# Kernel tuning notes

Measured on AMD Instinct MI355X. Metric: run time of the kernel, lower is better.

Reference implementation:

```python
import jax, jax.numpy as jnp
import numpy as np

BATCH = 4096
LATENT = 2048
ZDIM = 128
TEMP = 0.5
PRIOR = 0.3
PRIOR_PRIME = 0.5
GAMMA = 1.0
BETA = 0.0
EPS = 1e-8  # torch CosineSimilarity eps


def setup_inputs() -> dict:
    key = jax.random.key(0)
    k = jax.random.split(key, 6)
    return {
        "h_i": jax.random.normal(k[0], (BATCH, LATENT), dtype=jnp.float32),
        "h_j": jax.random.normal(k[1], (BATCH, LATENT), dtype=jnp.float32),
        "z_i": jax.random.normal(k[2], (BATCH, ZDIM), dtype=jnp.float32),
        "z_j": jax.random.normal(k[3], (BATCH, ZDIM), dtype=jnp.float32),
        "target": jax.random.randint(k[4], (BATCH, 1), 0, 2, dtype=jnp.int64 if jax.config.jax_enable_x64 else jnp.int32),
        "W": jax.random.normal(k[5], (1, LATENT), dtype=jnp.float32) * (1.0 / np.sqrt(LATENT)),
        "b": jnp.zeros((1,), dtype=jnp.float32),
        "weight_onnpu": jnp.asarray(0.5, dtype=jnp.float32),
    }


def _onnpu_loss(inp, target):
    # inp: [B, 1] classifier logit; target: [B, 1] in {0, 1} -> {-1, +1}
    t = (target * 2 - 1).astype(inp.dtype)
    positive = (t == 1).astype(inp.dtype)
    unlabeled = (t == -1).astype(inp.dtype)
    one = jnp.asarray(1.0, inp.dtype)
    n_pos = jnp.maximum(one, jnp.sum(positive))
    n_unl = jnp.maximum(one, jnp.sum(unlabeled))
    sig = jax.nn.sigmoid  # loss(x) = sigmoid(-x)
    y_pos = sig(-(positive * inp)) * positive
    y_pos_inv = sig(positive * inp) * positive
    y_unl = sig(unlabeled * inp) * unlabeled
    positive_risk = PRIOR_PRIME / n_pos * jnp.sum(y_pos)
    negative_risk = ((1.0 - PRIOR_PRIME) / (n_unl * (1.0 - PRIOR)) * jnp.sum(y_unl)
                     - (1.0 - PRIOR_PRIME) * PRIOR / (n_pos * (1.0 - PRIOR)) * jnp.sum(y_pos_inv))
    # nnPU correction (nnPU=True, beta=0, gamma=1)
    return jnp.where(negative_risk < -BETA, -GAMMA * negative_risk,
                     positive_risk + negative_risk)


def _nt_xent_loss(z_i, z_j):
    B = z_i.shape[0]
    N = 2 * B
    z = jnp.concatenate([z_i, z_j], axis=0)  # [N, D]
    zn = z / jnp.maximum(jnp.linalg.norm(z, axis=1, keepdims=True), EPS)
    sim = (zn @ zn.T) / TEMP  # [N, N] cosine similarity / temperature
    idx = jnp.arange(N)
    pos = sim[idx, (idx + B) % N]  # positive pair logit per row
    # CE over [positive | all-other-than-self]: denominator is logsumexp over
    # the row with the self-similarity (diagonal) excluded.
    sim_masked = jnp.where(idx[:, None] == idx[None, :], -jnp.inf, sim)
    lse = jax.nn.logsumexp(sim_masked, axis=1)
    return jnp.sum(lse - pos) / N


def reference(h_i, h_j, z_i, z_j, target, W, b, weight_onnpu):
    logit_i = h_i @ W.T + b  # [B, 1]
    logit_j = h_j @ W.T + b
    onnpu_l = 0.5 * (_onnpu_loss(logit_i, target) + _onnpu_loss(logit_j, target))
    nt_xent_l = _nt_xent_loss(z_i, z_j)
    return weight_onnpu * onnpu_l + (1.0 - weight_onnpu) * nt_xent_l
```

## Files before the change

### kernel.cpp

```cpp
#include <hip/hip_runtime.h>

#define BATCH  4096
#define NROWS  8192
#define LATENT 2048
#define ZDIM   128
#define PRIORc       0.3f
#define PRIOR_PRIMEc 0.5f

typedef __attribute__((ext_vector_type(8))) short bf16x8;
typedef __attribute__((ext_vector_type(4))) float f32x4;

__device__ inline unsigned short f2bf_rne(float f) {
    unsigned int u = __float_as_uint(f);
    u = u + 0x7fffu + ((u >> 16) & 1u);
    return (unsigned short)(u >> 16);
}

__device__ inline float wave_reduce_sum(float v) {
#pragma unroll
    for (int m = 1; m < 64; m <<= 1) v += __shfl_xor(v, m, 64);
    return v;
}

#define ZSCALE 1.69864464f

__global__ void k_prep(const float* __restrict__ z_i, const float* __restrict__ z_j,
                       const float* __restrict__ h_i, const float* __restrict__ h_j,
                       const float* __restrict__ W, const float* __restrict__ bb,
                       unsigned short* __restrict__ znb, float* __restrict__ pos,
                       float* __restrict__ dexp, float* __restrict__ S_row,
                       float* __restrict__ logits) {
    int bid = blockIdx.x;
    int wave = threadIdx.x >> 6, lane = threadIdx.x & 63;
    if (bid < 1024) {
        if (threadIdx.x < 8) S_row[bid * 8 + threadIdx.x] = 0.f;
        int r = bid * 4 + wave;
        int p = r + BATCH;
        float2 a = ((const float2*)(z_i + (size_t)r * ZDIM))[lane];
        float2 c = ((const float2*)(z_j + (size_t)r * ZDIM))[lane];
        float sa = wave_reduce_sum(a.x * a.x + a.y * a.y);
        float sc = wave_reduce_sum(c.x * c.x + c.y * c.y);
        float dd = wave_reduce_sum(a.x * c.x + a.y * c.y);
        float inva = 1.f / fmaxf(sqrtf(sa), 1e-8f);
        float invc = 1.f / fmaxf(sqrtf(sc), 1e-8f);
        if (lane == 0) {
            float pv = 2.0f * dd * inva * invc;
            pos[r] = pv;
            pos[p] = pv;
        }
        int kt = lane >> 4;
        int q  = (lane >> 2) & 3;
        int j  = (lane & 3) * 2;
        int lrow = q * 16;
        float fa = inva * ZSCALE, fc = invc * ZSCALE;
        ushort2 wa; wa.x = f2bf_rne(a.x * fa); wa.y = f2bf_rne(a.y * fa);
        ushort2 wc; wc.x = f2bf_rne(c.x * fc); wc.y = f2bf_rne(c.y * fc);
        {
            size_t off = ((size_t)((r >> 4) * 4 + kt) * 64 + (lrow + (r & 15))) * 8 + j;
            *(ushort2*)(znb + off) = wa;
        }
        {
            size_t off = ((size_t)((p >> 4) * 4 + kt) * 64 + (lrow + (p & 15))) * 8 + j;
            *(ushort2*)(znb + off) = wc;
        }
        float ax = __uint_as_float((unsigned)wa.x << 16);
        float ay = __uint_as_float((unsigned)wa.y << 16);
        float cx = __uint_as_float((unsigned)wc.x << 16);
        float cy = __uint_as_float((unsigned)wc.y << 16);
        float da = wave_reduce_sum(ax * ax + ay * ay);
        float dc = wave_reduce_sum(cx * cx + cy * cy);
        if (lane == 0) {
            dexp[r] = __builtin_amdgcn_exp2f(da);
            dexp[p] = __builtin_amdgcn_exp2f(dc);
        }
    } else {
        int r = (bid - 1024) * 4 + wave;
        const float* h = (r < BATCH) ? (h_i + (size_t)r * LATENT)
                                     : (h_j + (size_t)(r - BATCH) * LATENT);
        const f32x4* h4 = (const f32x4*)h;
        const f32x4* w4 = (const f32x4*)W;
        float s = 0.f;
#pragma unroll
        for (int itr = 0; itr < 8; ++itr) {
            f32x4 av = h4[itr * 64 + lane];
            f32x4 wv = w4[itr * 64 + lane];
            s += av.x * wv.x + av.y * wv.y + av.z * wv.z + av.w * wv.w;
        }
        s = wave_reduce_sum(s);
        if (lane == 0) logits[r] = s + bb[0];
    }
}

__global__ void __launch_bounds__(256, 3) k_sim(
        const unsigned short* __restrict__ znb, float* __restrict__ S_row) {
    int sid = blockIdx.x;
    int lane = threadIdx.x & 63, wave = threadIdx.x >> 6;
    int q = lane >> 4, t = lane & 15;
    int row0 = (sid & 63) * 128 + (wave >> 1) * 64;
    int gA = row0 >> 4;
    const bf16x8* zf = (const bf16x8*)znb;

    bf16x8 a[4][4];
#pragma unroll
    for (int mt = 0; mt < 4; ++mt)
#pragma unroll
        for (int kt = 0; kt < 4; ++kt)
            a[mt][kt] = zf[(size_t)((gA + mt) * 4 + kt) * 64 + lane];

    float s[16];
#pragma unroll
    for (int i = 0; i < 16; ++i) s[i] = 0.f;

    int colbase = (sid >> 6) * 512 + (wave & 1) * 64;
    int cb4 = colbase >> 4;
    bf16x8 b[4];
#pragma unroll
    for (int kt = 0; kt < 4; ++kt)
        b[kt] = zf[(size_t)(cb4 * 4 + kt) * 64 + lane];

#pragma unroll 1
    for (int it = 0; it < 4; ++it) {
#pragma unroll
        for (int nt = 0; nt < 4; ++nt) {
            bf16x8 bn[4];
            if (!(it == 3 && nt == 3)) {
                int ng = cb4 + (nt == 3 ? (it + 1) * 8 : it * 8 + nt + 1);
#pragma unroll
                for (int kt = 0; kt < 4; ++kt)
                    bn[kt] = zf[(size_t)(ng * 4 + kt) * 64 + lane];
            }
            f32x4 acc[4];
            f32x4 zero = {0.f, 0.f, 0.f, 0.f};
#pragma unroll
            for (int mt = 0; mt < 4; ++mt) acc[mt] = zero;
#pragma unroll
            for (int kt = 0; kt < 4; ++kt)
#pragma unroll
                for (int mt = 0; mt < 4; ++mt)
                    acc[mt] = __builtin_amdgcn_mfma_f32_16x16x32_bf16(a[mt][kt], b[kt], acc[mt], 0, 0, 0);
#pragma unroll
            for (int mt = 0; mt < 4; ++mt)
#pragma unroll
                for (int reg = 0; reg < 4; ++reg)
                    s[mt * 4 + reg] += __builtin_amdgcn_exp2f(acc[mt][reg]);
#pragma unroll
            for (int kt = 0; kt < 4; ++kt) b[kt] = bn[kt];
        }
    }
#pragma unroll
    for (int i = 0; i < 16; ++i) {
        float v = s[i];
        v += __shfl_xor(v, 1, 64);
        v += __shfl_xor(v, 2, 64);
        v += __shfl_xor(v, 4, 64);
        v += __shfl_xor(v, 8, 64);
        if (t == 0) atomicAdd(&S_row[row0 + (i >> 2) * 16 + q * 4 + (i & 3)], v);
    }
}

__global__ void k_final(const float* __restrict__ S_row, const float* __restrict__ pos,
                        const float* __restrict__ dexp, const float* __restrict__ logits,
                        const int* __restrict__ target,
                        const float* __restrict__ w_onnpu, float* __restrict__ out) {
    float nt_s = 0.f;
    for (int r = threadIdx.x; r < NROWS; r += 1024)
        nt_s += __logf(S_row[r] - dexp[r]) - pos[r];
    float v[8];
#pragma unroll
    for (int i = 0; i < 8; ++i) v[i] = 0.f;
    for (int r = threadIdx.x; r < BATCH; r += 1024) {
        float li = logits[r], lj = logits[BATCH + r];
        bool p = (target[r] == 1);
        float si_n = 1.f / (1.f + __expf(li));
        float si_p = 1.f / (1.f + __expf(-li));
        float sj_n = 1.f / (1.f + __expf(lj));
        float sj_p = 1.f / (1.f + __expf(-lj));
        v[0] += p ? 1.f : 0.f;
        v[1] += p ? 0.f : 1.f;
        v[2] += p ? si_n : 0.f;
        v[3] += p ? si_p : 0.f;
        v[4] += p ? 0.f : si_p;
        v[5] += p ? sj_n : 0.f;
        v[6] += p ? sj_p : 0.f;
        v[7] += p ? 0.f : sj_p;
    }
    __shared__ float red[16][9];
    int wave = threadIdx.x >> 6, lane = threadIdx.x & 63;
    nt_s = wave_reduce_sum(nt_s);
#pragma unroll
    for (int i = 0; i < 8; ++i) v[i] = wave_reduce_sum(v[i]);
    if (lane == 0) {
        red[wave][0] = nt_s;
#pragma unroll
        for (int i = 0; i < 8; ++i) red[wave][1 + i] = v[i];
    }
    __syncthreads();
    if (threadIdx.x == 0) {
        float t[9];
#pragma unroll
        for (int i = 0; i < 9; ++i) {
            float acc = 0.f;
#pragma unroll
            for (int wv = 0; wv < 16; ++wv) acc += red[wv][i];
            t[i] = acc;
        }
        float ntxent = t[0] / (float)NROWS;
        float np = fmaxf(1.f, t[1]), nu = fmaxf(1.f, t[2]);
        float pr_i = PRIOR_PRIMEc / np * t[3];
        float nr_i = (1.f - PRIOR_PRIMEc) / (nu * (1.f - PRIORc)) * t[5]
                   - (1.f - PRIOR_PRIMEc) * PRIORc / (np * (1.f - PRIORc)) * t[4];
        float li_loss = (nr_i < 0.f) ? -nr_i : (pr_i + nr_i);
        float pr_j = PRIOR_PRIMEc / np * t[6];
        float nr_j = (1.f - PRIOR_PRIMEc) / (nu * (1.f - PRIORc)) * t[8]
                   - (1.f - PRIOR_PRIMEc) * PRIORc / (np * (1.f - PRIORc)) * t[7];
        float lj_loss = (nr_j < 0.f) ? -nr_j : (pr_j + nr_j);
        float onnpu = 0.5f * (li_loss + lj_loss);
        float w = w_onnpu[0];
        out[0] = w * onnpu + (1.f - w) * ntxent;
    }
}

extern "C" void kernel_launch(void* const* d_in, const int* in_sizes, int n_in,
                              void* d_out, int out_size, void* d_ws, size_t ws_size,
                              hipStream_t stream) {
    const float* h_i = (const float*)d_in[0];
    const float* h_j = (const float*)d_in[1];
    const float* z_i = (const float*)d_in[2];
    const float* z_j = (const float*)d_in[3];
    const int* target = (const int*)d_in[4];
    const float* W = (const float*)d_in[5];
    const float* b = (const float*)d_in[6];
    const float* w_onnpu = (const float*)d_in[7];

    char* ws = (char*)d_ws;
    unsigned short* znb = (unsigned short*)ws;
    float* S_row  = (float*)(ws + 2097152);
    float* pos    = (float*)(ws + 2097152 + 32768);
    float* logits = (float*)(ws + 2097152 + 65536);
    float* dexp   = (float*)(ws + 2097152 + 98304);
    float* out = (float*)d_out;

    k_prep<<<3072, 256, 0, stream>>>(z_i, z_j, h_i, h_j, W, b, znb, pos, dexp, S_row, logits);
    k_sim<<<1024, 256, 0, stream>>>(znb, S_row);
    k_final<<<1, 1024, 0, stream>>>(S_row, pos, dexp, logits, target, w_onnpu, out);
}
```

Measured before the change: 147.6 us.

## Exploit similarity matrix symmetry by computing only upper-triangular tiles

The similarity kernel is remapped so each block handles one 128x128 tile of the upper triangle, 2080 tiles in total, instead of 128x512 strips covering the full matrix. Each off-diagonal tile adds its exp-sums to both the row sums and the column sums, which roughly halves the MFMA and exp2 work. Partial sums are combined in shared memory before global atomics. In exchange there are more, smaller blocks, a triangular index decode with a square root, extra LDS atomics and a block barrier, and twice as many global atomics per tile.

```diff
diff --git a/kernel.cpp b/kernel.cpp
--- a/kernel.cpp
+++ b/kernel.cpp
@@ -93,12 +93,25 @@
 
 __global__ void __launch_bounds__(256, 3) k_sim(
         const unsigned short* __restrict__ znb, float* __restrict__ S_row) {
-    int sid = blockIdx.x;
+    int k = blockIdx.x;
+    int i = (int)((129.0f - sqrtf(16641.0f - 8.0f * (float)k)) * 0.5f);
+    if (i > 63) i = 63;
+    while (i * (129 - i) / 2 > k) --i;
+    while ((i + 1) * (128 - i) / 2 <= k) ++i;
+    int j = i + (k - i * (129 - i) / 2);
+    bool diag = (i == j);
+
     int lane = threadIdx.x & 63, wave = threadIdx.x >> 6;
     int q = lane >> 4, t = lane & 15;
-    int row0 = (sid & 63) * 128 + (wave >> 1) * 64;
+    int row0 = i * 128 + (wave >> 1) * 64;
+    int colbase = j * 128 + (wave & 1) * 64;
     int gA = row0 >> 4;
+    int cb4 = colbase >> 4;
     const bf16x8* zf = (const bf16x8*)znb;
+
+    __shared__ float red[256];
+    red[threadIdx.x] = 0.f;
+    __syncthreads();
 
     bf16x8 a[4][4];
 #pragma unroll
@@ -107,54 +120,72 @@
         for (int kt = 0; kt < 4; ++kt)
             a[mt][kt] = zf[(size_t)((gA + mt) * 4 + kt) * 64 + lane];
 
-    float s[16];
-#pragma unroll
-    for (int i = 0; i < 16; ++i) s[i] = 0.f;
-
-    int colbase = (sid >> 6) * 512 + (wave & 1) * 64;
-    int cb4 = colbase >> 4;
     bf16x8 b[4];
 #pragma unroll
     for (int kt = 0; kt < 4; ++kt)
         b[kt] = zf[(size_t)(cb4 * 4 + kt) * 64 + lane];
 
-#pragma unroll 1
-    for (int it = 0; it < 4; ++it) {
-#pragma unroll
-        for (int nt = 0; nt < 4; ++nt) {
-            bf16x8 bn[4];
-            if (!(it == 3 && nt == 3)) {
-                int ng = cb4 + (nt == 3 ? (it + 1) * 8 : it * 8 + nt + 1);
-#pragma unroll
-                for (int kt = 0; kt < 4; ++kt)
-                    bn[kt] = zf[(size_t)(ng * 4 + kt) * 64 + lane];
+    float s[16];
+#pragma unroll
+    for (int idx = 0; idx < 16; ++idx) s[idx] = 0.f;
+    float c[4];
+
+#pragma unroll
+    for (int nt = 0; nt < 4; ++nt) {
+        bf16x8 bn[4];
+        if (nt < 3) {
+#pragma unroll
+            for (int kt = 0; kt < 4; ++kt)
+                bn[kt] = zf[(size_t)((cb4 + nt + 1) * 4 + kt) * 64 + lane];
+        }
+        f32x4 acc[4];
+        f32x4 zero = {0.f, 0.f, 0.f, 0.f};
+#pragma unroll
+        for (int mt = 0; mt < 4; ++mt) acc[mt] = zero;
+#pragma unroll
+        for (int kt = 0; kt < 4; ++kt)
+#pragma unroll
+            for (int mt = 0; mt < 4; ++mt)
+                acc[mt] = __builtin_amdgcn_mfma_f32_16x16x32_bf16(a[mt][kt], b[kt], acc[mt], 0, 0, 0);
+        float csum = 0.f;
+#pragma unroll
+        for (int mt = 0; mt < 4; ++mt)
+#pragma unroll
+            for (int reg = 0; reg < 4; ++reg) {
+                float e = __builtin_amdgcn_exp2f(acc[mt][reg]);
+                s[mt * 4 + reg] += e;
+                csum += e;
             }
-            f32x4 acc[4];
-            f32x4 zero = {0.f, 0.f, 0.f, 0.f};
-#pragma unroll
-            for (int mt = 0; mt < 4; ++mt) acc[mt] = zero;
-#pragma unroll
-            for (int kt = 0; kt < 4; ++kt)
-#pragma unroll
-                for (int mt = 0; mt < 4; ++mt)
-                    acc[mt] = __builtin_amdgcn_mfma_f32_16x16x32_bf16(a[mt][kt], b[kt], acc[mt], 0, 0, 0);
-#pragma unroll
-            for (int mt = 0; mt < 4; ++mt)
-#pragma unroll
-                for (int reg = 0; reg < 4; ++reg)
-                    s[mt * 4 + reg] += __builtin_amdgcn_exp2f(acc[mt][reg]);
+        c[nt] = csum;
+        if (nt < 3) {
 #pragma unroll
             for (int kt = 0; kt < 4; ++kt) b[kt] = bn[kt];
         }
     }
-#pragma unroll
-    for (int i = 0; i < 16; ++i) {
-        float v = s[i];
+
+#pragma unroll
+    for (int idx = 0; idx < 16; ++idx) {
+        float v = s[idx];
         v += __shfl_xor(v, 1, 64);
         v += __shfl_xor(v, 2, 64);
         v += __shfl_xor(v, 4, 64);
         v += __shfl_xor(v, 8, 64);
-        if (t == 0) atomicAdd(&S_row[row0 + (i >> 2) * 16 + q * 4 + (i & 3)], v);
+        if (t == 0)
+            atomicAdd(&red[(wave >> 1) * 64 + (idx >> 2) * 16 + q * 4 + (idx & 3)], v);
+    }
+#pragma unroll
+    for (int nt = 0; nt < 4; ++nt) {
+        float v = c[nt];
+        v += __shfl_xor(v, 16, 64);
+        v += __shfl_xor(v, 32, 64);
+        if (q == 0)
+            atomicAdd(&red[128 + (wave & 1) * 64 + nt * 16 + t], v);
+    }
+    __syncthreads();
+    if (threadIdx.x < 128) {
+        atomicAdd(&S_row[i * 128 + threadIdx.x], red[threadIdx.x]);
+    } else if (!diag) {
+        atomicAdd(&S_row[j * 128 + (threadIdx.x & 127)], red[threadIdx.x]);
     }
 }
 
@@ -241,6 +272,6 @@
     float* out = (float*)d_out;
 
     k_prep<<<3072, 256, 0, stream>>>(z_i, z_j, h_i, h_j, W, b, znb, pos, dexp, S_row, logits);
-    k_sim<<<1024, 256, 0, stream>>>(znb, S_row);
+    k_sim<<<2080, 256, 0, stream>>>(znb, S_row);
     k_final<<<1, 1024, 0, stream>>>(S_row, pos, dexp, logits, target, w_onnpu, out);
 }
```

After: 137.1 us. 1.08x faster.
